# Performance work log

Measured on AMD Instinct MI355X. Metric: run time of the kernel, lower is better.

## Reference

```python
import jax, jax.numpy as jnp
import numpy as np

N_NODES = 50000
N_EDGES = 800000
N_FEAT = 128
HID = 128
N_LAYER = 3
FC_HID = 256
N_CLASS = 10
N_GRAPHS = 64


def setup_inputs() -> dict:
    key = jax.random.key(0)
    ks = jax.random.split(key, 10)
    x = jax.random.normal(ks[0], (N_NODES, N_FEAT), dtype=jnp.float32)
    edge_index = jax.random.randint(ks[1], (2, N_EDGES), 0, N_NODES, dtype=jnp.int32)
    batch = jnp.sort(jax.random.randint(ks[2], (N_NODES,), 0, N_GRAPHS, dtype=jnp.int32))
    s = 0.05
    # SAGEConv per layer: lin_l acts on mean-aggregated neighbors, lin_r on root.
    Wl = jax.random.normal(ks[3], (N_LAYER, HID, HID), dtype=jnp.float32) * s
    Wr = jax.random.normal(ks[4], (N_LAYER, HID, HID), dtype=jnp.float32) * s
    bl = jnp.zeros((N_LAYER, HID), dtype=jnp.float32)
    fc1_w = jax.random.normal(ks[5], (HID * N_LAYER, FC_HID), dtype=jnp.float32) * s
    fc1_b = jnp.zeros((FC_HID,), dtype=jnp.float32)
    fc2_w = jax.random.normal(ks[6], (FC_HID, N_CLASS), dtype=jnp.float32) * s
    fc2_b = jnp.zeros((N_CLASS,), dtype=jnp.float32)
    return {"x": x, "edge_index": edge_index, "batch": batch,
            "Wl": Wl, "Wr": Wr, "bl": bl,
            "fc1_w": fc1_w, "fc1_b": fc1_b, "fc2_w": fc2_w, "fc2_b": fc2_b}


def reference(x, edge_index, batch, Wl, Wr, bl, fc1_w, fc1_b, fc2_w, fc2_b):
    # normalize edge indices to start at 0 (as in the torch forward)
    ei = edge_index - jnp.min(edge_index)
    src, dst = ei[0], ei[1]
    # in-degree for mean aggregation (clamped to avoid div-by-zero)
    deg = jax.ops.segment_sum(jnp.ones((src.shape[0],), x.dtype), dst,
                              num_segments=N_NODES)
    inv_deg = 1.0 / jnp.maximum(deg, 1.0)[:, None]  # [N,1]
    h = x
    layer_outs = []
    for i in range(N_LAYER):
        # (dropout is identity in eval mode)
        agg = jax.ops.segment_sum(h[src], dst, num_segments=N_NODES) * inv_deg  # [N,H]
        h = jax.nn.relu(agg @ Wl[i] + h @ Wr[i] + bl[i])
        layer_outs.append(h)
    hcat = jnp.concatenate(layer_outs, axis=1)  # [N, H*n_layer]
    # mean pooling per graph
    counts = jax.ops.segment_sum(jnp.ones((N_NODES,), x.dtype), batch,
                                 num_segments=N_GRAPHS)
    pooled = jax.ops.segment_sum(hcat, batch, num_segments=N_GRAPHS)
    pooled = pooled / jnp.maximum(counts, 1.0)[:, None]  # [G, H*n_layer]
    out = jax.nn.relu(pooled @ fc1_w + fc1_b) @ fc2_w + fc2_b  # [G, n_class]
    return out
```

## Files before the change

kernel.cpp:

```cpp
#include <hip/hip_runtime.h>
#include <hip/hip_bf16.h>
#include <limits.h>

#define N_NODES 50000
#define N_EDGES 800000
#define HID 128
#define N_LAYER 3
#define FC_HID 256
#define N_CLASS 10
#define N_GRAPHS 64
#define NBKT 98
#define BIN_NB 256
#define PER_BLK ((N_EDGES + BIN_NB - 1) / BIN_NB)
#define CVT_NB ((N_NODES * HID / 4 + 255) / 256)

typedef __attribute__((ext_vector_type(8))) short short8;
typedef __attribute__((ext_vector_type(4))) float f32x4;

__device__ inline unsigned f2bf(float f) {
    unsigned u = __float_as_uint(f);
    return (u + 0x7FFFu + ((u >> 16) & 1u)) >> 16;
}
__device__ inline float bf2f(unsigned b) { return __uint_as_float(b << 16); }

__global__ __launch_bounds__(512) void k_minh(const int* __restrict__ ei,
                                              int* __restrict__ bmin,
                                              int* __restrict__ hist) {
    __shared__ int red[512];
    __shared__ int lh[NBKT];
    int t = threadIdx.x;
    if (t < NBKT) lh[t] = 0;
    __syncthreads();
    int e0 = blockIdx.x * PER_BLK, e1 = min(e0 + PER_BLK, N_EDGES);
    int v = INT_MAX;
    for (int j = e0 + t; j < e1; j += 512) {
        int s = ei[j], d = ei[N_EDGES + j];
        v = min(v, min(s, d));
        atomicAdd(&lh[d >> 9], 1);
    }
    red[t] = v;
    __syncthreads();
    for (int off = 256; off > 0; off >>= 1) {
        if (t < off) red[t] = min(red[t], red[t + off]);
        __syncthreads();
    }
    if (t == 0) bmin[blockIdx.x] = red[0];
    if (t < NBKT) hist[blockIdx.x * NBKT + t] = lh[t];
}

__global__ void k_base(const int* __restrict__ hist, int* __restrict__ colex,
                       int* __restrict__ btot, float* __restrict__ pooled) {
    __shared__ int s[BIN_NB];
    int b = blockIdx.x, t = threadIdx.x;
    int gid = b * BIN_NB + t;
    if (gid < N_GRAPHS * HID * N_LAYER) pooled[gid] = 0.f;
    int v = hist[t * NBKT + b];
    s[t] = v;
    __syncthreads();
    for (int off = 1; off < BIN_NB; off <<= 1) {
        int u = (t >= off) ? s[t - off] : 0;
        __syncthreads();
        s[t] += u;
        __syncthreads();
    }
    colex[t * NBKT + b] = s[t] - v;
    if (t == BIN_NB - 1) btot[b] = s[t];
}

__global__ void k_bscan(const int* __restrict__ btot, const int* __restrict__ bmin,
                        int* __restrict__ bboff, int* __restrict__ rp,
                        int* __restrict__ emin, const int* __restrict__ batch,
                        float* __restrict__ counts) {
    __shared__ int s[128];
    __shared__ int s2[128];
    int t = threadIdx.x;
    s2[t] = min(bmin[t], bmin[t + 128]);
    __syncthreads();
    for (int off = 64; off > 0; off >>= 1) {
        if (t < off) s2[t] = min(s2[t], s2[t + off]);
        __syncthreads();
    }
    if (t == 0) *emin = s2[0];
    int v = (t < NBKT) ? btot[t] : 0;
    s[t] = v;
    __syncthreads();
    for (int off = 1; off < 128; off <<= 1) {
        int u = (t >= off) ? s[t - off] : 0;
        __syncthreads();
        s[t] += u;
        __syncthreads();
    }
    if (t < NBKT) bboff[t] = s[t] - v;
    if (t == 127) { bboff[NBKT] = s[127]; rp[N_NODES] = s[127]; }
    if (t < N_GRAPHS) {
        int g = t;
        int lo = 0, hi = N_NODES;
        while (lo < hi) { int mid = (lo + hi) >> 1; if (batch[mid] < g) lo = mid + 1; else hi = mid; }
        int lb = lo;
        lo = lb; hi = N_NODES;
        while (lo < hi) { int mid = (lo + hi) >> 1; if (batch[mid] <= g) lo = mid + 1; else hi = mid; }
        counts[g] = (float)(lo - lb);
    }
}

__global__ __launch_bounds__(512) void k_bin(const int* __restrict__ ei,
                                             const int* __restrict__ emin,
                                             const int* __restrict__ bboff,
                                             const int* __restrict__ colex,
                                             unsigned* __restrict__ ebuf) {
    __shared__ int lcnt[NBKT];
    __shared__ int lbase[NBKT];
    int t = threadIdx.x, blk = blockIdx.x;
    if (t < NBKT) {
        lcnt[t] = 0;
        lbase[t] = bboff[t] + colex[blk * NBKT + t];
    }
    __syncthreads();
    int m = *emin;
    int e0 = blk * PER_BLK, e1 = min(e0 + PER_BLK, N_EDGES);
    for (int j = e0 + t; j < e1; j += 512) {
        int s = ei[j] - m, d = ei[N_EDGES + j];
        int bk = d >> 9;
        int idx = atomicAdd(&lcnt[bk], 1);
        ebuf[lbase[bk] + idx] = ((unsigned)s << 9) | (unsigned)(d & 511);
    }
}

__global__ __launch_bounds__(512) void k_scatter2(const unsigned* __restrict__ ebuf,
                                                  const int* __restrict__ bboff,
                                                  const int* __restrict__ emin,
                                                  int* __restrict__ rp,
                                                  float* __restrict__ invd,
                                                  int* __restrict__ csr) {
    __shared__ int ldeg[512];
    __shared__ int lsc[512];
    __shared__ int lfill[512];
    int b = blockIdx.x, t = threadIdx.x;
    int m = *emin;
    if (b == NBKT) {
        for (int nd = NBKT * 512 - m + t; nd < N_NODES; nd += 512)
            if (nd >= 0) { rp[nd] = N_EDGES; invd[nd] = 1.0f; }
        return;
    }
    ldeg[t] = 0;
    lfill[t] = 0;
    __syncthreads();
    int beg = bboff[b], end = bboff[b + 1];
    for (int e = beg + t; e < end; e += 512)
        atomicAdd(&ldeg[ebuf[e] & 511], 1);
    __syncthreads();
    int v = ldeg[t];
    lsc[t] = v;
    __syncthreads();
    for (int off = 1; off < 512; off <<= 1) {
        int u = (t >= off) ? lsc[t - off] : 0;
        __syncthreads();
        lsc[t] += u;
        __syncthreads();
    }
    int base = beg + lsc[t] - v;
    lsc[t] = base;
    int nd = (b << 9) + t - m;
    if (nd >= 0 && nd < N_NODES) {
        rp[nd] = base;
        invd[nd] = 1.0f / (float)max(v, 1);
    }
    __syncthreads();
    for (int e = beg + t; e < end; e += 512) {
        unsigned p = ebuf[e];
        int loc = p & 511;
        int pos = lsc[loc] + atomicAdd(&lfill[loc], 1);
        csr[pos] = (int)(p >> 9);
    }
}

__global__ void k_cvtprep(const float* __restrict__ x, unsigned* __restrict__ xb,
                          const float* __restrict__ Wl, const float* __restrict__ Wr,
                          unsigned* __restrict__ wlh, unsigned* __restrict__ wll,
                          unsigned* __restrict__ wrh, unsigned* __restrict__ wrl) {
    int b = blockIdx.x, t = threadIdx.x;
    if (b < 6) {
        const float* src = (b < 3) ? (Wl + (size_t)b * HID * HID) : (Wr + (size_t)(b - 3) * HID * HID);
        unsigned* dh = (b < 3) ? (wlh + (size_t)b * HID * 64) : (wrh + (size_t)(b - 3) * HID * 64);
        unsigned* dl = (b < 3) ? (wll + (size_t)b * HID * 64) : (wrl + (size_t)(b - 3) * HID * 64);
        for (int i = 0; i < 32; ++i) {
            int u = t * 32 + i;
            int n = u >> 6, kk = u & 63;
            float v0 = src[(size_t)(2 * kk) * HID + n];
            float v1 = src[(size_t)(2 * kk + 1) * HID + n];
            unsigned h0 = f2bf(v0), h1 = f2bf(v1);
            unsigned l0 = f2bf(v0 - bf2f(h0)), l1 = f2bf(v1 - bf2f(h1));
            dh[u] = h0 | (h1 << 16);
            dl[u] = l0 | (l1 << 16);
        }
    } else {
        int i = (b - 6) * 256 + t;
        if (i < N_NODES * HID / 4) {
            float4 v = *(const float4*)(x + (size_t)i * 4);
            uint2 o;
            o.x = f2bf(v.x) | (f2bf(v.y) << 16);
            o.y = f2bf(v.z) | (f2bf(v.w) << 16);
            *(uint2*)(xb + (size_t)i * 2) = o;
        }
    }
}

__global__ void k_agg(const unsigned* __restrict__ hb, const int* __restrict__ rp,
                      const int* __restrict__ csr, const float* __restrict__ invd,
                      unsigned* __restrict__ aggb) {
    const int n = blockIdx.x;
    const int lane = threadIdx.x;
    int beg = rp[n], end = rp[n + 1];
    float a0 = 0, a1 = 0, b0 = 0, b1 = 0, c0 = 0, c1 = 0, d0 = 0, d1 = 0;
    int e = beg;
    for (; e + 16 <= end; e += 16) {
        int s[16];
        unsigned u[16];
#pragma unroll
        for (int i = 0; i < 16; ++i) s[i] = csr[e + i];
#pragma unroll
        for (int i = 0; i < 16; ++i) u[i] = hb[(size_t)s[i] * 64 + lane];
#pragma unroll
        for (int i = 0; i < 16; i += 4) {
            a0 += __uint_as_float(u[i] << 16);     a1 += __uint_as_float(u[i] & 0xFFFF0000u);
            b0 += __uint_as_float(u[i + 1] << 16); b1 += __uint_as_float(u[i + 1] & 0xFFFF0000u);
            c0 += __uint_as_float(u[i + 2] << 16); c1 += __uint_as_float(u[i + 2] & 0xFFFF0000u);
            d0 += __uint_as_float(u[i + 3] << 16); d1 += __uint_as_float(u[i + 3] & 0xFFFF0000u);
        }
    }
    for (; e + 4 <= end; e += 4) {
        int s0 = csr[e], s1 = csr[e + 1], s2 = csr[e + 2], s3 = csr[e + 3];
        unsigned u0 = hb[(size_t)s0 * 64 + lane];
        unsigned u1 = hb[(size_t)s1 * 64 + lane];
        unsigned u2 = hb[(size_t)s2 * 64 + lane];
        unsigned u3 = hb[(size_t)s3 * 64 + lane];
        a0 += __uint_as_float(u0 << 16); a1 += __uint_as_float(u0 & 0xFFFF0000u);
        b0 += __uint_as_float(u1 << 16); b1 += __uint_as_float(u1 & 0xFFFF0000u);
        c0 += __uint_as_float(u2 << 16); c1 += __uint_as_float(u2 & 0xFFFF0000u);
        d0 += __uint_as_float(u3 << 16); d1 += __uint_as_float(u3 & 0xFFFF0000u);
    }
    for (; e < end; ++e) {
        unsigned u = hb[(size_t)csr[e] * 64 + lane];
        a0 += __uint_as_float(u << 16);
        a1 += __uint_as_float(u & 0xFFFF0000u);
    }
    float iv = invd[n];
    unsigned o = f2bf((a0 + b0 + c0 + d0) * iv) | (f2bf((a1 + b1 + c1 + d1) * iv) << 16);
    aggb[(size_t)n * 64 + lane] = o;
}

__global__ __launch_bounds__(256, 4) void k_gemm(
    const unsigned* __restrict__ aggb, const unsigned* __restrict__ hinb,
    const unsigned* __restrict__ wlh, const unsigned* __restrict__ wll,
    const unsigned* __restrict__ wrh, const unsigned* __restrict__ wrl,
    const float* __restrict__ bias, const int* __restrict__ batch,
    unsigned* __restrict__ houtb, float* __restrict__ pooled, int layer) {
    __shared__ float Ts[64 * 132];
    __shared__ int bs[64];
    const int tx = threadIdx.x;
    const int wave = tx >> 6, lane = tx & 63;
    const int row0 = blockIdx.x * 64;
    const int lrow = lane & 15, kgrp = lane >> 4;

    if (tx < 64) {
        int grow = row0 + tx;
        bs[tx] = (grow < N_NODES) ? batch[grow] : -1;
    }

    f32x4 acc[4][2];
#pragma unroll
    for (int m = 0; m < 4; ++m)
#pragma unroll
        for (int n = 0; n < 2; ++n) acc[m][n] = (f32x4){0.f, 0.f, 0.f, 0.f};
    const short8 zf = {0, 0, 0, 0, 0, 0, 0, 0};

    for (int kc = 0; kc < 4; ++kc) {
        const int koff = kc * 16 + kgrp * 4;
        short8 af[4], hf[4];
#pragma unroll
        for (int m = 0; m < 4; ++m) {
            int r = row0 + m * 16 + lrow;
            if (r < N_NODES) {
                af[m] = *(const short8*)(aggb + (size_t)r * 64 + koff);
                hf[m] = *(const short8*)(hinb + (size_t)r * 64 + koff);
            } else {
                af[m] = zf;
                hf[m] = zf;
            }
        }
#pragma unroll
        for (int n = 0; n < 2; ++n) {
            int wn = wave * 2 + n;
            size_t wbase = (size_t)(wn * 16 + lrow) * 64 + koff;
            short8 fl_h = *(const short8*)(wlh + wbase);
            short8 fl_l = *(const short8*)(wll + wbase);
            short8 fr_h = *(const short8*)(wrh + wbase);
            short8 fr_l = *(const short8*)(wrl + wbase);
#pragma unroll
            for (int m = 0; m < 4; ++m) {
                acc[m][n] = __builtin_amdgcn_mfma_f32_16x16x32_bf16(af[m], fl_h, acc[m][n], 0, 0, 0);
                acc[m][n] = __builtin_amdgcn_mfma_f32_16x16x32_bf16(af[m], fl_l, acc[m][n], 0, 0, 0);
                acc[m][n] = __builtin_amdgcn_mfma_f32_16x16x32_bf16(hf[m], fr_h, acc[m][n], 0, 0, 0);
                acc[m][n] = __builtin_amdgcn_mfma_f32_16x16x32_bf16(hf[m], fr_l, acc[m][n], 0, 0, 0);
            }
        }
    }

#pragma unroll
    for (int n = 0; n < 2; ++n) {
        int c = wave * 32 + n * 16 + lrow;
        float bb = bias[c];
#pragma unroll
        for (int m = 0; m < 4; ++m)
#pragma unroll
            for (int reg = 0; reg < 4; ++reg) {
                int r = m * 16 + kgrp * 4 + reg;
                Ts[r * 132 + c] = fmaxf(acc[m][n][reg] + bb, 0.f);
            }
    }
    __syncthreads();

#pragma unroll
    for (int it = 0; it < 4; ++it) {
        int f = it * 256 + tx;
        int r = f >> 4, slot = f & 15;
        int grow = row0 + r;
        if (grow < N_NODES) {
            const float* ts = &Ts[r * 132 + slot * 8];
            uint4 o;
            o.x = f2bf(ts[0]) | (f2bf(ts[1]) << 16);
            o.y = f2bf(ts[2]) | (f2bf(ts[3]) << 16);
            o.z = f2bf(ts[4]) | (f2bf(ts[5]) << 16);
            o.w = f2bf(ts[6]) | (f2bf(ts[7]) << 16);
            *(uint4*)(houtb + (size_t)grow * 64 + slot * 4) = o;
        }
    }

    {
        int j = tx & 127, half = tx >> 7;
        int rbeg = half * 32, rend = rbeg + 32;
        float run = 0.f;
        int curb = bs[rbeg];
        for (int r = rbeg; r < rend; ++r) {
            int bb = bs[r];
            if (bb != curb) {
                if (curb >= 0)
                    atomicAdd(&pooled[(size_t)curb * (HID * N_LAYER) + layer * HID + j], run);
                run = 0.f;
                curb = bb;
            }
            run += Ts[r * 132 + j];
        }
        if (curb >= 0)
            atomicAdd(&pooled[(size_t)curb * (HID * N_LAYER) + layer * HID + j], run);
    }
}

__global__ void k_fc(const float* __restrict__ pooled, const float* __restrict__ counts,
                     const float* __restrict__ fc1w, const float* __restrict__ fc1b,
                     const float* __restrict__ fc2w, const float* __restrict__ fc2b,
                     float* __restrict__ out) {
    __shared__ float pr[HID * N_LAYER];
    __shared__ float a1[FC_HID];
    const int g = blockIdx.x, t = threadIdx.x;
    float invc = 1.0f / fmaxf(counts[g], 1.0f);
    for (int i = t; i < HID * N_LAYER; i += FC_HID)
        pr[i] = pooled[(size_t)g * (HID * N_LAYER) + i] * invc;
    __syncthreads();
    float acc = fc1b[t];
    for (int k = 0; k < HID * N_LAYER; ++k)
        acc = fmaf(pr[k], fc1w[(size_t)k * FC_HID + t], acc);
    a1[t] = fmaxf(acc, 0.f);
    __syncthreads();
    if (t < N_CLASS) {
        float o = fc2b[t];
        for (int k = 0; k < FC_HID; ++k)
            o = fmaf(a1[k], fc2w[(size_t)k * N_CLASS + t], o);
        out[(size_t)g * N_CLASS + t] = o;
    }
}

extern "C" void kernel_launch(void* const* d_in, const int* in_sizes, int n_in,
                              void* d_out, int out_size, void* d_ws, size_t ws_size,
                              hipStream_t stream) {
    const float* x = (const float*)d_in[0];
    const int* ei = (const int*)d_in[1];
    const int* batch = (const int*)d_in[2];
    const float* Wl = (const float*)d_in[3];
    const float* Wr = (const float*)d_in[4];
    const float* bl = (const float*)d_in[5];
    const float* fc1w = (const float*)d_in[6];
    const float* fc1b = (const float*)d_in[7];
    const float* fc2w = (const float*)d_in[8];
    const float* fc2b = (const float*)d_in[9];
    float* out = (float*)d_out;

    char* ws = (char*)d_ws;
    size_t off = 0;
    auto alloc = [&](size_t bytes) {
        void* p = ws + off;
        off += (bytes + 255) & ~size_t(255);
        return p;
    };
    int* emin = (int*)alloc(4);
    int* bmin = (int*)alloc(BIN_NB * 4);
    float* pooled = (float*)alloc((size_t)N_GRAPHS * HID * N_LAYER * 4);
    int* hist = (int*)alloc((size_t)BIN_NB * NBKT * 4);
    int* colex = (int*)alloc((size_t)BIN_NB * NBKT * 4);
    int* btot = (int*)alloc(NBKT * 4);
    int* bboff = (int*)alloc((NBKT + 1) * 4);
    int* rp = (int*)alloc((N_NODES + 1) * 4);
    float* invd = (float*)alloc(N_NODES * 4);
    float* counts = (float*)alloc(N_GRAPHS * 4);
    unsigned* ebuf = (unsigned*)alloc((size_t)N_EDGES * 4);
    int* csr = (int*)alloc((size_t)N_EDGES * 4);
    unsigned* wlh = (unsigned*)alloc((size_t)N_LAYER * HID * 64 * 4);
    unsigned* wll = (unsigned*)alloc((size_t)N_LAYER * HID * 64 * 4);
    unsigned* wrh = (unsigned*)alloc((size_t)N_LAYER * HID * 64 * 4);
    unsigned* wrl = (unsigned*)alloc((size_t)N_LAYER * HID * 64 * 4);
    unsigned* aggb = (unsigned*)alloc((size_t)N_NODES * 64 * 4);
    unsigned* xb = (unsigned*)alloc((size_t)N_NODES * 64 * 4);
    unsigned* hb1 = (unsigned*)alloc((size_t)N_NODES * 64 * 4);
    unsigned* hb2 = (unsigned*)alloc((size_t)N_NODES * 64 * 4);

    k_minh<<<BIN_NB, 512, 0, stream>>>(ei, bmin, hist);
    k_base<<<NBKT, BIN_NB, 0, stream>>>(hist, colex, btot, pooled);
    k_bscan<<<1, 128, 0, stream>>>(btot, bmin, bboff, rp, emin, batch, counts);
    k_bin<<<BIN_NB, 512, 0, stream>>>(ei, emin, bboff, colex, ebuf);
    k_scatter2<<<NBKT + 1, 512, 0, stream>>>(ebuf, bboff, emin, rp, invd, csr);
    k_cvtprep<<<6 + CVT_NB, 256, 0, stream>>>(x, xb, Wl, Wr, wlh, wll, wrh, wrl);

    const unsigned* hin = xb;
    unsigned* houts[3] = {hb1, hb2, hb1};
    for (int layer = 0; layer < N_LAYER; ++layer) {
        k_agg<<<N_NODES, 64, 0, stream>>>(hin, rp, csr, invd, aggb);
        k_gemm<<<(N_NODES + 63) / 64, 256, 0, stream>>>(
            aggb, hin,
            wlh + (size_t)layer * HID * 64, wll + (size_t)layer * HID * 64,
            wrh + (size_t)layer * HID * 64, wrl + (size_t)layer * HID * 64,
            bl + (size_t)layer * HID, batch, houts[layer], pooled, layer);
        hin = houts[layer];
    }
    k_fc<<<N_GRAPHS, 256, 0, stream>>>(pooled, counts, fc1w, fc1b, fc2w, fc2b, out);
}
```

Baseline: 255.4 us.

## Fuse CSR build and input conversion into one cooperative kernel with grid syncs

Replaces six separate preprocessing launches (min/histogram, base scan, bucket scan, binning, scatter, bf16 conversion) with a single cooperative kernel that uses grid-wide syncs between phases. The x and weight conversion are folded into the first phase to overlap with the histogram work. This targets launch overhead and idle gaps between small kernels, at the cost of grid-sync barriers and a fixed 256-block grid. The old launch path is kept as a fallback if the cooperative launch fails.

```diff
diff --git a/kernel.cpp b/kernel.cpp
--- a/kernel.cpp
+++ b/kernel.cpp
@@ -1,6 +1,9 @@
 #include <hip/hip_runtime.h>
 #include <hip/hip_bf16.h>
+#include <hip/hip_cooperative_groups.h>
 #include <limits.h>
+
+namespace cg = cooperative_groups;
 
 #define N_NODES 50000
 #define N_EDGES 800000
@@ -22,6 +25,193 @@
     return (u + 0x7FFFu + ((u >> 16) & 1u)) >> 16;
 }
 __device__ inline float bf2f(unsigned b) { return __uint_as_float(b << 16); }
+
+__device__ inline void wprep_one(const float* __restrict__ src, unsigned* __restrict__ dh,
+                                 unsigned* __restrict__ dl, int t, int per) {
+    for (int i = 0; i < per; ++i) {
+        int u = t * per + i;
+        int n = u >> 6, kk = u & 63;
+        float v0 = src[(size_t)(2 * kk) * HID + n];
+        float v1 = src[(size_t)(2 * kk + 1) * HID + n];
+        unsigned h0 = f2bf(v0), h1 = f2bf(v1);
+        unsigned l0 = f2bf(v0 - bf2f(h0)), l1 = f2bf(v1 - bf2f(h1));
+        dh[u] = h0 | (h1 << 16);
+        dl[u] = l0 | (l1 << 16);
+    }
+}
+
+__global__ __launch_bounds__(512) void k_prep_all(
+    const int* __restrict__ ei, const float* __restrict__ x,
+    const float* __restrict__ Wl, const float* __restrict__ Wr,
+    unsigned* __restrict__ xb,
+    unsigned* __restrict__ wlh, unsigned* __restrict__ wll,
+    unsigned* __restrict__ wrh, unsigned* __restrict__ wrl,
+    float* __restrict__ pooled, int* __restrict__ bmin, int* __restrict__ hist,
+    int* __restrict__ colex, int* __restrict__ btot, int* __restrict__ bboff,
+    int* __restrict__ rp, int* __restrict__ emin, const int* __restrict__ batch,
+    float* __restrict__ counts, unsigned* __restrict__ ebuf,
+    float* __restrict__ invd, int* __restrict__ csr) {
+    cg::grid_group grid = cg::this_grid();
+    __shared__ int sm[1536];
+    const int b = blockIdx.x, t = threadIdx.x;
+
+    {
+        int gid = b * 512 + t;
+        if (gid < N_GRAPHS * HID * N_LAYER) pooled[gid] = 0.f;
+        for (int i = gid; i < N_NODES * HID / 4; i += BIN_NB * 512) {
+            float4 v = *(const float4*)(x + (size_t)i * 4);
+            uint2 o;
+            o.x = f2bf(v.x) | (f2bf(v.y) << 16);
+            o.y = f2bf(v.z) | (f2bf(v.w) << 16);
+            *(uint2*)(xb + (size_t)i * 2) = o;
+        }
+        if (b >= 250) {
+            int w = b - 250;
+            const float* src = (w < 3) ? (Wl + (size_t)w * HID * HID)
+                                       : (Wr + (size_t)(w - 3) * HID * HID);
+            unsigned* dh = (w < 3) ? (wlh + (size_t)w * HID * 64) : (wrh + (size_t)(w - 3) * HID * 64);
+            unsigned* dl = (w < 3) ? (wll + (size_t)w * HID * 64) : (wrl + (size_t)(w - 3) * HID * 64);
+            wprep_one(src, dh, dl, t, 16);
+        }
+    }
+
+    {
+        int* red = sm;
+        int* lh = sm + 512;
+        if (t < NBKT) lh[t] = 0;
+        __syncthreads();
+        int e0 = b * PER_BLK, e1 = min(e0 + PER_BLK, N_EDGES);
+        int v = INT_MAX;
+        for (int j = e0 + t; j < e1; j += 512) {
+            int s = ei[j], d = ei[N_EDGES + j];
+            v = min(v, min(s, d));
+            atomicAdd(&lh[d >> 9], 1);
+        }
+        red[t] = v;
+        __syncthreads();
+        for (int off = 256; off > 0; off >>= 1) {
+            if (t < off) red[t] = min(red[t], red[t + off]);
+            __syncthreads();
+        }
+        if (t == 0) bmin[b] = red[0];
+        if (t < NBKT) hist[b * NBKT + t] = lh[t];
+    }
+    __threadfence();
+    grid.sync();
+
+    if (b < NBKT) {
+        int* s = sm;
+        int v = 0;
+        if (t < BIN_NB) { v = hist[t * NBKT + b]; s[t] = v; }
+        __syncthreads();
+        for (int off = 1; off < BIN_NB; off <<= 1) {
+            int u = (t >= off && t < BIN_NB) ? s[t - off] : 0;
+            __syncthreads();
+            if (t < BIN_NB) s[t] += u;
+            __syncthreads();
+        }
+        if (t < BIN_NB) colex[t * NBKT + b] = s[t] - v;
+        if (t == BIN_NB - 1) btot[b] = s[t];
+    }
+    __threadfence();
+    grid.sync();
+
+    if (b == 0) {
+        int* s = sm;
+        int* s2 = sm + 128;
+        if (t < 128) s2[t] = min(bmin[t], bmin[t + 128]);
+        __syncthreads();
+        for (int off = 64; off > 0; off >>= 1) {
+            if (t < off) s2[t] = min(s2[t], s2[t + off]);
+            __syncthreads();
+        }
+        if (t == 0) *emin = s2[0];
+        int v = (t < NBKT) ? btot[t] : 0;
+        if (t < 128) s[t] = v;
+        __syncthreads();
+        for (int off = 1; off < 128; off <<= 1) {
+            int u = (t >= off && t < 128) ? s[t - off] : 0;
+            __syncthreads();
+            if (t < 128) s[t] += u;
+            __syncthreads();
+        }
+        if (t < NBKT) bboff[t] = s[t] - v;
+        if (t == 127) { bboff[NBKT] = s[127]; rp[N_NODES] = s[127]; }
+        if (t < N_GRAPHS) {
+            int g = t;
+            int lo = 0, hi = N_NODES;
+            while (lo < hi) { int mid = (lo + hi) >> 1; if (batch[mid] < g) lo = mid + 1; else hi = mid; }
+            int lb = lo;
+            lo = lb; hi = N_NODES;
+            while (lo < hi) { int mid = (lo + hi) >> 1; if (batch[mid] <= g) lo = mid + 1; else hi = mid; }
+            counts[g] = (float)(lo - lb);
+        }
+    }
+    __threadfence();
+    grid.sync();
+
+    {
+        int* lcnt = sm;
+        int* lbase = sm + 128;
+        if (t < NBKT) {
+            lcnt[t] = 0;
+            lbase[t] = bboff[t] + colex[b * NBKT + t];
+        }
+        __syncthreads();
+        int m = *emin;
+        int e0 = b * PER_BLK, e1 = min(e0 + PER_BLK, N_EDGES);
+        for (int j = e0 + t; j < e1; j += 512) {
+            int s = ei[j] - m, d = ei[N_EDGES + j];
+            int bk = d >> 9;
+            int idx = atomicAdd(&lcnt[bk], 1);
+            ebuf[lbase[bk] + idx] = ((unsigned)s << 9) | (unsigned)(d & 511);
+        }
+    }
+    __threadfence();
+    grid.sync();
+
+    if (b <= NBKT) {
+        int m = *emin;
+        if (b == NBKT) {
+            for (int nd = NBKT * 512 - m + t; nd < N_NODES; nd += 512)
+                if (nd >= 0) { rp[nd] = N_EDGES; invd[nd] = 1.0f; }
+        } else {
+            int* ldeg = sm;
+            int* lsc = sm + 512;
+            int* lfill = sm + 1024;
+            ldeg[t] = 0;
+            lfill[t] = 0;
+            __syncthreads();
+            int beg = bboff[b], end = bboff[b + 1];
+            for (int e = beg + t; e < end; e += 512)
+                atomicAdd(&ldeg[ebuf[e] & 511], 1);
+            __syncthreads();
+            int v = ldeg[t];
+            lsc[t] = v;
+            __syncthreads();
+            for (int off = 1; off < 512; off <<= 1) {
+                int u = (t >= off) ? lsc[t - off] : 0;
+                __syncthreads();
+                lsc[t] += u;
+                __syncthreads();
+            }
+            int base = beg + lsc[t] - v;
+            lsc[t] = base;
+            int nd = (b << 9) + t - m;
+            if (nd >= 0 && nd < N_NODES) {
+                rp[nd] = base;
+                invd[nd] = 1.0f / (float)max(v, 1);
+            }
+            __syncthreads();
+            for (int e = beg + t; e < end; e += 512) {
+                unsigned p = ebuf[e];
+                int loc = p & 511;
+                int pos = lsc[loc] + atomicAdd(&lfill[loc], 1);
+                csr[pos] = (int)(p >> 9);
+            }
+        }
+    }
+}
 
 __global__ __launch_bounds__(512) void k_minh(const int* __restrict__ ei,
                                               int* __restrict__ bmin,
@@ -183,16 +373,7 @@
         const float* src = (b < 3) ? (Wl + (size_t)b * HID * HID) : (Wr + (size_t)(b - 3) * HID * HID);
         unsigned* dh = (b < 3) ? (wlh + (size_t)b * HID * 64) : (wrh + (size_t)(b - 3) * HID * 64);
         unsigned* dl = (b < 3) ? (wll + (size_t)b * HID * 64) : (wrl + (size_t)(b - 3) * HID * 64);
-        for (int i = 0; i < 32; ++i) {
-            int u = t * 32 + i;
-            int n = u >> 6, kk = u & 63;
-            float v0 = src[(size_t)(2 * kk) * HID + n];
-            float v1 = src[(size_t)(2 * kk + 1) * HID + n];
-            unsigned h0 = f2bf(v0), h1 = f2bf(v1);
-            unsigned l0 = f2bf(v0 - bf2f(h0)), l1 = f2bf(v1 - bf2f(h1));
-            dh[u] = h0 | (h1 << 16);
-            dl[u] = l0 | (l1 << 16);
-        }
+        wprep_one(src, dh, dl, t, 32);
     } else {
         int i = (b - 6) * 256 + t;
         if (i < N_NODES * HID / 4) {
@@ -423,12 +604,31 @@
     unsigned* hb1 = (unsigned*)alloc((size_t)N_NODES * 64 * 4);
     unsigned* hb2 = (unsigned*)alloc((size_t)N_NODES * 64 * 4);
 
-    k_minh<<<BIN_NB, 512, 0, stream>>>(ei, bmin, hist);
-    k_base<<<NBKT, BIN_NB, 0, stream>>>(hist, colex, btot, pooled);
-    k_bscan<<<1, 128, 0, stream>>>(btot, bmin, bboff, rp, emin, batch, counts);
-    k_bin<<<BIN_NB, 512, 0, stream>>>(ei, emin, bboff, colex, ebuf);
-    k_scatter2<<<NBKT + 1, 512, 0, stream>>>(ebuf, bboff, emin, rp, invd, csr);
-    k_cvtprep<<<6 + CVT_NB, 256, 0, stream>>>(x, xb, Wl, Wr, wlh, wll, wrh, wrl);
+    {
+        const int* ei_p = ei; const float* x_p = x;
+        const float* Wl_p = Wl; const float* Wr_p = Wr;
+        unsigned* xb_p = xb;
+        unsigned* wlh_p = wlh; unsigned* wll_p = wll;
+        unsigned* wrh_p = wrh; unsigned* wrl_p = wrl;
+        float* pooled_p = pooled; int* bmin_p = bmin; int* hist_p = hist;
+        int* colex_p = colex; int* btot_p = btot; int* bboff_p = bboff;
+        int* rp_p = rp; int* emin_p = emin; const int* batch_p = batch;
+        float* counts_p = counts; unsigned* ebuf_p = ebuf;
+        float* invd_p = invd; int* csr_p = csr;
+        void* args[] = {&ei_p, &x_p, &Wl_p, &Wr_p, &xb_p, &wlh_p, &wll_p, &wrh_p, &wrl_p,
+                        &pooled_p, &bmin_p, &hist_p, &colex_p, &btot_p, &bboff_p,
+                        &rp_p, &emin_p, &batch_p, &counts_p, &ebuf_p, &invd_p, &csr_p};
+        hipError_t err = hipLaunchCooperativeKernel((const void*)k_prep_all, dim3(BIN_NB),
+                                                    dim3(512), args, 0, stream);
+        if (err != hipSuccess) {
+            k_minh<<<BIN_NB, 512, 0, stream>>>(ei, bmin, hist);
+            k_base<<<NBKT, BIN_NB, 0, stream>>>(hist, colex, btot, pooled);
+            k_bscan<<<1, 128, 0, stream>>>(btot, bmin, bboff, rp, emin, batch, counts);
+            k_bin<<<BIN_NB, 512, 0, stream>>>(ei, emin, bboff, colex, ebuf);
+            k_scatter2<<<NBKT + 1, 512, 0, stream>>>(ebuf, bboff, emin, rp, invd, csr);
+            k_cvtprep<<<6 + CVT_NB, 256, 0, stream>>>(x, xb, Wl, Wr, wlh, wll, wrh, wrl);
+        }
+    }
 
     const unsigned* hin = xb;
     unsigned* houts[3] = {hb1, hb2, hb1};
```

New measurement: 544.4 us. 113% more time.

## Fold preprocessing kernels together and skip final layer hidden-state store

Applied to the files above, without the earlier changes.

Merges the x/weight bf16 conversion into the edge min/histogram kernel. It also removes the single-block bucket-scan kernel: the min reduction and graph counts move into k_base, and each block of k_bin and k_scatter2 recomputes the bucket prefix sum redundantly. The last GEMM layer no longer writes its bf16 hidden output, since only the pooled sums are consumed afterwards. This cuts two kernel launches and one full hidden-state write, at the cost of redundant small scans per block and a heavier first kernel.

```diff
diff --git a/kernel.cpp b/kernel.cpp
--- a/kernel.cpp
+++ b/kernel.cpp
@@ -12,7 +12,6 @@
 #define NBKT 98
 #define BIN_NB 256
 #define PER_BLK ((N_EDGES + BIN_NB - 1) / BIN_NB)
-#define CVT_NB ((N_NODES * HID / 4 + 255) / 256)
 
 typedef __attribute__((ext_vector_type(8))) short short8;
 typedef __attribute__((ext_vector_type(4))) float f32x4;
@@ -23,35 +22,65 @@
 }
 __device__ inline float bf2f(unsigned b) { return __uint_as_float(b << 16); }
 
-__global__ __launch_bounds__(512) void k_minh(const int* __restrict__ ei,
-                                              int* __restrict__ bmin,
-                                              int* __restrict__ hist) {
+__global__ __launch_bounds__(512) void k_minh(
+    const int* __restrict__ ei, const float* __restrict__ x,
+    const float* __restrict__ Wl, const float* __restrict__ Wr,
+    int* __restrict__ bmin, int* __restrict__ hist, unsigned* __restrict__ xb,
+    unsigned* __restrict__ wlh, unsigned* __restrict__ wll,
+    unsigned* __restrict__ wrh, unsigned* __restrict__ wrl) {
     __shared__ int red[512];
     __shared__ int lh[NBKT];
-    int t = threadIdx.x;
+    const int b = blockIdx.x, t = threadIdx.x;
     if (t < NBKT) lh[t] = 0;
     __syncthreads();
-    int e0 = blockIdx.x * PER_BLK, e1 = min(e0 + PER_BLK, N_EDGES);
+    int e0 = b * PER_BLK, e1 = min(e0 + PER_BLK, N_EDGES);
     int v = INT_MAX;
     for (int j = e0 + t; j < e1; j += 512) {
         int s = ei[j], d = ei[N_EDGES + j];
         v = min(v, min(s, d));
         atomicAdd(&lh[d >> 9], 1);
     }
+    for (int i = b * 512 + t; i < N_NODES * HID / 4; i += BIN_NB * 512) {
+        float4 xv = *(const float4*)(x + (size_t)i * 4);
+        uint2 o;
+        o.x = f2bf(xv.x) | (f2bf(xv.y) << 16);
+        o.y = f2bf(xv.z) | (f2bf(xv.w) << 16);
+        *(uint2*)(xb + (size_t)i * 2) = o;
+    }
+    if (b >= 250) {
+        int w = b - 250;
+        const float* src = (w < 3) ? (Wl + (size_t)w * HID * HID)
+                                   : (Wr + (size_t)(w - 3) * HID * HID);
+        unsigned* dh = (w < 3) ? (wlh + (size_t)w * HID * 64) : (wrh + (size_t)(w - 3) * HID * 64);
+        unsigned* dl = (w < 3) ? (wll + (size_t)w * HID * 64) : (wrl + (size_t)(w - 3) * HID * 64);
+        for (int i = 0; i < 16; ++i) {
+            int u = t * 16 + i;
+            int n = u >> 6, kk = u & 63;
+            float v0 = src[(size_t)(2 * kk) * HID + n];
+            float v1 = src[(size_t)(2 * kk + 1) * HID + n];
+            unsigned h0 = f2bf(v0), h1 = f2bf(v1);
+            unsigned l0 = f2bf(v0 - bf2f(h0)), l1 = f2bf(v1 - bf2f(h1));
+            dh[u] = h0 | (h1 << 16);
+            dl[u] = l0 | (l1 << 16);
+        }
+    }
     red[t] = v;
     __syncthreads();
     for (int off = 256; off > 0; off >>= 1) {
         if (t < off) red[t] = min(red[t], red[t + off]);
         __syncthreads();
     }
-    if (t == 0) bmin[blockIdx.x] = red[0];
-    if (t < NBKT) hist[blockIdx.x * NBKT + t] = lh[t];
+    if (t == 0) bmin[b] = red[0];
+    if (t < NBKT) hist[b * NBKT + t] = lh[t];
 }
 
 __global__ void k_base(const int* __restrict__ hist, int* __restrict__ colex,
-                       int* __restrict__ btot, float* __restrict__ pooled) {
+                       int* __restrict__ btot, float* __restrict__ pooled,
+                       const int* __restrict__ bmin, int* __restrict__ emin,
+                       const int* __restrict__ batch, float* __restrict__ counts) {
     __shared__ int s[BIN_NB];
-    int b = blockIdx.x, t = threadIdx.x;
+    __shared__ int s2[BIN_NB];
+    const int b = blockIdx.x, t = threadIdx.x;
     int gid = b * BIN_NB + t;
     if (gid < N_GRAPHS * HID * N_LAYER) pooled[gid] = 0.f;
     int v = hist[t * NBKT + b];
@@ -65,55 +94,47 @@
     }
     colex[t * NBKT + b] = s[t] - v;
     if (t == BIN_NB - 1) btot[b] = s[t];
-}
-
-__global__ void k_bscan(const int* __restrict__ btot, const int* __restrict__ bmin,
-                        int* __restrict__ bboff, int* __restrict__ rp,
-                        int* __restrict__ emin, const int* __restrict__ batch,
-                        float* __restrict__ counts) {
-    __shared__ int s[128];
-    __shared__ int s2[128];
-    int t = threadIdx.x;
-    s2[t] = min(bmin[t], bmin[t + 128]);
-    __syncthreads();
-    for (int off = 64; off > 0; off >>= 1) {
-        if (t < off) s2[t] = min(s2[t], s2[t + off]);
-        __syncthreads();
-    }
-    if (t == 0) *emin = s2[0];
-    int v = (t < NBKT) ? btot[t] : 0;
-    s[t] = v;
-    __syncthreads();
-    for (int off = 1; off < 128; off <<= 1) {
-        int u = (t >= off) ? s[t - off] : 0;
-        __syncthreads();
-        s[t] += u;
-        __syncthreads();
-    }
-    if (t < NBKT) bboff[t] = s[t] - v;
-    if (t == 127) { bboff[NBKT] = s[127]; rp[N_NODES] = s[127]; }
-    if (t < N_GRAPHS) {
-        int g = t;
-        int lo = 0, hi = N_NODES;
-        while (lo < hi) { int mid = (lo + hi) >> 1; if (batch[mid] < g) lo = mid + 1; else hi = mid; }
-        int lb = lo;
-        lo = lb; hi = N_NODES;
-        while (lo < hi) { int mid = (lo + hi) >> 1; if (batch[mid] <= g) lo = mid + 1; else hi = mid; }
-        counts[g] = (float)(lo - lb);
+    if (b == 0) {
+        s2[t] = bmin[t];
+        __syncthreads();
+        for (int off = 128; off > 0; off >>= 1) {
+            if (t < off) s2[t] = min(s2[t], s2[t + off]);
+            __syncthreads();
+        }
+        if (t == 0) *emin = s2[0];
+        if (t < N_GRAPHS) {
+            int g = t;
+            int lo = 0, hi = N_NODES;
+            while (lo < hi) { int mid = (lo + hi) >> 1; if (batch[mid] < g) lo = mid + 1; else hi = mid; }
+            int lb = lo;
+            lo = lb; hi = N_NODES;
+            while (lo < hi) { int mid = (lo + hi) >> 1; if (batch[mid] <= g) lo = mid + 1; else hi = mid; }
+            counts[g] = (float)(lo - lb);
+        }
     }
 }
 
 __global__ __launch_bounds__(512) void k_bin(const int* __restrict__ ei,
                                              const int* __restrict__ emin,
-                                             const int* __restrict__ bboff,
+                                             const int* __restrict__ btot,
                                              const int* __restrict__ colex,
                                              unsigned* __restrict__ ebuf) {
+    __shared__ int sb[128];
     __shared__ int lcnt[NBKT];
     __shared__ int lbase[NBKT];
-    int t = threadIdx.x, blk = blockIdx.x;
+    const int t = threadIdx.x, blk = blockIdx.x;
+    int v = (t < NBKT) ? btot[t] : 0;
+    if (t < 128) sb[t] = v;
+    __syncthreads();
+    for (int off = 1; off < 128; off <<= 1) {
+        int u = (t >= off && t < 128) ? sb[t - off] : 0;
+        __syncthreads();
+        if (t < 128) sb[t] += u;
+        __syncthreads();
+    }
     if (t < NBKT) {
         lcnt[t] = 0;
-        lbase[t] = bboff[t] + colex[blk * NBKT + t];
+        lbase[t] = (sb[t] - v) + colex[blk * NBKT + t];
     }
     __syncthreads();
     int m = *emin;
@@ -127,7 +148,7 @@
 }
 
 __global__ __launch_bounds__(512) void k_scatter2(const unsigned* __restrict__ ebuf,
-                                                  const int* __restrict__ bboff,
+                                                  const int* __restrict__ btot,
                                                   const int* __restrict__ emin,
                                                   int* __restrict__ rp,
                                                   float* __restrict__ invd,
@@ -135,22 +156,36 @@
     __shared__ int ldeg[512];
     __shared__ int lsc[512];
     __shared__ int lfill[512];
-    int b = blockIdx.x, t = threadIdx.x;
+    __shared__ int bbsh[NBKT + 1];
+    const int b = blockIdx.x, t = threadIdx.x;
+    int v = (t < NBKT) ? btot[t] : 0;
+    if (t < 128) ldeg[t] = v;
+    __syncthreads();
+    for (int off = 1; off < 128; off <<= 1) {
+        int u = (t >= off && t < 128) ? ldeg[t - off] : 0;
+        __syncthreads();
+        if (t < 128) ldeg[t] += u;
+        __syncthreads();
+    }
+    if (t < NBKT) bbsh[t] = ldeg[t] - v;
+    if (t == 127) bbsh[NBKT] = ldeg[127];
+    __syncthreads();
     int m = *emin;
     if (b == NBKT) {
+        if (t == 0) rp[N_NODES] = bbsh[NBKT];
         for (int nd = NBKT * 512 - m + t; nd < N_NODES; nd += 512)
             if (nd >= 0) { rp[nd] = N_EDGES; invd[nd] = 1.0f; }
         return;
     }
+    int beg = bbsh[b], end = bbsh[b + 1];
     ldeg[t] = 0;
     lfill[t] = 0;
     __syncthreads();
-    int beg = bboff[b], end = bboff[b + 1];
     for (int e = beg + t; e < end; e += 512)
         atomicAdd(&ldeg[ebuf[e] & 511], 1);
     __syncthreads();
-    int v = ldeg[t];
-    lsc[t] = v;
+    int dv = ldeg[t];
+    lsc[t] = dv;
     __syncthreads();
     for (int off = 1; off < 512; off <<= 1) {
         int u = (t >= off) ? lsc[t - off] : 0;
@@ -158,12 +193,12 @@
         lsc[t] += u;
         __syncthreads();
     }
-    int base = beg + lsc[t] - v;
+    int base = beg + lsc[t] - dv;
     lsc[t] = base;
     int nd = (b << 9) + t - m;
     if (nd >= 0 && nd < N_NODES) {
         rp[nd] = base;
-        invd[nd] = 1.0f / (float)max(v, 1);
+        invd[nd] = 1.0f / (float)max(dv, 1);
     }
     __syncthreads();
     for (int e = beg + t; e < end; e += 512) {
@@ -171,37 +206,6 @@
         int loc = p & 511;
         int pos = lsc[loc] + atomicAdd(&lfill[loc], 1);
         csr[pos] = (int)(p >> 9);
-    }
-}
-
-__global__ void k_cvtprep(const float* __restrict__ x, unsigned* __restrict__ xb,
-                          const float* __restrict__ Wl, const float* __restrict__ Wr,
-                          unsigned* __restrict__ wlh, unsigned* __restrict__ wll,
-                          unsigned* __restrict__ wrh, unsigned* __restrict__ wrl) {
-    int b = blockIdx.x, t = threadIdx.x;
-    if (b < 6) {
-        const float* src = (b < 3) ? (Wl + (size_t)b * HID * HID) : (Wr + (size_t)(b - 3) * HID * HID);
-        unsigned* dh = (b < 3) ? (wlh + (size_t)b * HID * 64) : (wrh + (size_t)(b - 3) * HID * 64);
-        unsigned* dl = (b < 3) ? (wll + (size_t)b * HID * 64) : (wrl + (size_t)(b - 3) * HID * 64);
-        for (int i = 0; i < 32; ++i) {
-            int u = t * 32 + i;
-            int n = u >> 6, kk = u & 63;
-            float v0 = src[(size_t)(2 * kk) * HID + n];
-            float v1 = src[(size_t)(2 * kk + 1) * HID + n];
-            unsigned h0 = f2bf(v0), h1 = f2bf(v1);
-            unsigned l0 = f2bf(v0 - bf2f(h0)), l1 = f2bf(v1 - bf2f(h1));
-            dh[u] = h0 | (h1 << 16);
-            dl[u] = l0 | (l1 << 16);
-        }
-    } else {
-        int i = (b - 6) * 256 + t;
-        if (i < N_NODES * HID / 4) {
-            float4 v = *(const float4*)(x + (size_t)i * 4);
-            uint2 o;
-            o.x = f2bf(v.x) | (f2bf(v.y) << 16);
-            o.y = f2bf(v.z) | (f2bf(v.w) << 16);
-            *(uint2*)(xb + (size_t)i * 2) = o;
-        }
     }
 }
 
@@ -254,7 +258,7 @@
     const unsigned* __restrict__ wlh, const unsigned* __restrict__ wll,
     const unsigned* __restrict__ wrh, const unsigned* __restrict__ wrl,
     const float* __restrict__ bias, const int* __restrict__ batch,
-    unsigned* __restrict__ houtb, float* __restrict__ pooled, int layer) {
+    unsigned* __restrict__ houtb, float* __restrict__ pooled, int layer, int store_h) {
     __shared__ float Ts[64 * 132];
     __shared__ int bs[64];
     const int tx = threadIdx.x;
@@ -320,19 +324,21 @@
     }
     __syncthreads();
 
-#pragma unroll
-    for (int it = 0; it < 4; ++it) {
-        int f = it * 256 + tx;
-        int r = f >> 4, slot = f & 15;
-        int grow = row0 + r;
-        if (grow < N_NODES) {
-            const float* ts = &Ts[r * 132 + slot * 8];
-            uint4 o;
-            o.x = f2bf(ts[0]) | (f2bf(ts[1]) << 16);
-            o.y = f2bf(ts[2]) | (f2bf(ts[3]) << 16);
-            o.z = f2bf(ts[4]) | (f2bf(ts[5]) << 16);
-            o.w = f2bf(ts[6]) | (f2bf(ts[7]) << 16);
-            *(uint4*)(houtb + (size_t)grow * 64 + slot * 4) = o;
+    if (store_h) {
+#pragma unroll
+        for (int it = 0; it < 4; ++it) {
+            int f = it * 256 + tx;
+            int r = f >> 4, slot = f & 15;
+            int grow = row0 + r;
+            if (grow < N_NODES) {
+                const float* ts = &Ts[r * 132 + slot * 8];
+                uint4 o;
+                o.x = f2bf(ts[0]) | (f2bf(ts[1]) << 16);
+                o.y = f2bf(ts[2]) | (f2bf(ts[3]) << 16);
+                o.z = f2bf(ts[4]) | (f2bf(ts[5]) << 16);
+                o.w = f2bf(ts[6]) | (f2bf(ts[7]) << 16);
+                *(uint4*)(houtb + (size_t)grow * 64 + slot * 4) = o;
+            }
         }
     }
 
@@ -408,7 +414,6 @@
     int* hist = (int*)alloc((size_t)BIN_NB * NBKT * 4);
     int* colex = (int*)alloc((size_t)BIN_NB * NBKT * 4);
     int* btot = (int*)alloc(NBKT * 4);
-    int* bboff = (int*)alloc((NBKT + 1) * 4);
     int* rp = (int*)alloc((N_NODES + 1) * 4);
     float* invd = (float*)alloc(N_NODES * 4);
     float* counts = (float*)alloc(N_GRAPHS * 4);
@@ -423,12 +428,10 @@
     unsigned* hb1 = (unsigned*)alloc((size_t)N_NODES * 64 * 4);
     unsigned* hb2 = (unsigned*)alloc((size_t)N_NODES * 64 * 4);
 
-    k_minh<<<BIN_NB, 512, 0, stream>>>(ei, bmin, hist);
-    k_base<<<NBKT, BIN_NB, 0, stream>>>(hist, colex, btot, pooled);
-    k_bscan<<<1, 128, 0, stream>>>(btot, bmin, bboff, rp, emin, batch, counts);
-    k_bin<<<BIN_NB, 512, 0, stream>>>(ei, emin, bboff, colex, ebuf);
-    k_scatter2<<<NBKT + 1, 512, 0, stream>>>(ebuf, bboff, emin, rp, invd, csr);
-    k_cvtprep<<<6 + CVT_NB, 256, 0, stream>>>(x, xb, Wl, Wr, wlh, wll, wrh, wrl);
+    k_minh<<<BIN_NB, 512, 0, stream>>>(ei, x, Wl, Wr, bmin, hist, xb, wlh, wll, wrh, wrl);
+    k_base<<<NBKT, BIN_NB, 0, stream>>>(hist, colex, btot, pooled, bmin, emin, batch, counts);
+    k_bin<<<BIN_NB, 512, 0, stream>>>(ei, emin, btot, colex, ebuf);
+    k_scatter2<<<NBKT + 1, 512, 0, stream>>>(ebuf, btot, emin, rp, invd, csr);
 
     const unsigned* hin = xb;
     unsigned* houts[3] = {hb1, hb2, hb1};
@@ -438,7 +441,8 @@
             aggb, hin,
             wlh + (size_t)layer * HID * 64, wll + (size_t)layer * HID * 64,
             wrh + (size_t)layer * HID * 64, wrl + (size_t)layer * HID * 64,
-            bl + (size_t)layer * HID, batch, houts[layer], pooled, layer);
+            bl + (size_t)layer * HID, batch, houts[layer], pooled, layer,
+            layer < N_LAYER - 1 ? 1 : 0);
         hin = houts[layer];
     }
     k_fc<<<N_GRAPHS, 256, 0, stream>>>(pooled, counts, fc1w, fc1b, fc2w, fc2b, out);
```

New measurement: 249.4 us. 1.02x faster.
